# Performance work log

Hardware: AMD Instinct MI355X
Metric: run time of the kernel (lower is better)

## Reference

```python
import jax, jax.numpy as jnp
import numpy as np

N_NODES = 50000
N_EDGES = 800000
IN_DIM = 128
HID = 32
HEADS = 4
OUT_DIM = 128
NEG_SLOPE = 0.2


def setup_inputs() -> dict:
    key = jax.random.key(0)
    ks = jax.random.split(key, 10)
    s = lambda fan_in: 1.0 / np.sqrt(fan_in)
    return {
        "x": jax.random.normal(ks[0], (N_NODES, IN_DIM), dtype=jnp.float32),
        "edge_index": jax.random.randint(ks[1], (2, N_EDGES), 0, N_NODES, dtype=jnp.int64),
        # encoder GATConv: in=IN_DIM, out=HID, heads=HEADS (concat)
        "W1": jax.random.normal(ks[2], (IN_DIM, HEADS * HID), dtype=jnp.float32) * s(IN_DIM),
        "att_src1": jax.random.normal(ks[3], (HEADS, HID), dtype=jnp.float32) * s(HID),
        "att_dst1": jax.random.normal(ks[4], (HEADS, HID), dtype=jnp.float32) * s(HID),
        "b1": jnp.zeros((HEADS * HID,), dtype=jnp.float32),
        # decoder GATConv: in=HEADS*HID, out=OUT_DIM, heads=1
        "W2": jax.random.normal(ks[5], (HEADS * HID, OUT_DIM), dtype=jnp.float32) * s(HEADS * HID),
        "att_src2": jax.random.normal(ks[6], (1, OUT_DIM), dtype=jnp.float32) * s(OUT_DIM),
        "att_dst2": jax.random.normal(ks[7], (1, OUT_DIM), dtype=jnp.float32) * s(OUT_DIM),
        "b2": jnp.zeros((OUT_DIM,), dtype=jnp.float32),
    }


def _gat_conv(x, src, dst, W, att_src, att_dst, bias, heads, out_ch):
    """PyG-style GATConv (v1), eval mode (dropout off), self-loops already in src/dst."""
    n = x.shape[0]
    h = (x @ W).reshape(n, heads, out_ch)                 # [N,H,C]
    a_src = jnp.einsum("nhc,hc->nh", h, att_src)          # [N,H]
    a_dst = jnp.einsum("nhc,hc->nh", h, att_dst)          # [N,H]
    e = jax.nn.leaky_relu(a_src[src] + a_dst[dst], NEG_SLOPE)  # [E,H]
    # segment softmax over destination neighborhoods
    e_max = jax.ops.segment_max(e, dst, num_segments=n)   # [N,H]
    e_exp = jnp.exp(e - e_max[dst])
    denom = jax.ops.segment_sum(e_exp, dst, num_segments=n)
    alpha = e_exp / (denom[dst] + 1e-16)                  # [E,H]
    msg = h[src] * alpha[:, :, None]                      # [E,H,C]
    out = jax.ops.segment_sum(msg, dst, num_segments=n)   # [N,H,C]
    return out.reshape(n, heads * out_ch) + bias


def reference(x, edge_index, W1, att_src1, att_dst1, b1, W2, att_src2, att_dst2, b2):
    n = x.shape[0]
    loops = jnp.arange(n, dtype=edge_index.dtype)
    src = jnp.concatenate([edge_index[0], loops])
    dst = jnp.concatenate([edge_index[1], loops])
    z = jax.nn.relu(_gat_conv(x, src, dst, W1, att_src1, att_dst1, b1, HEADS, HID))
    x_hat = jax.nn.relu(_gat_conv(z, src, dst, W2, att_src2, att_dst2, b2, 1, OUT_DIM))
    return x_hat
```

## Files before the change

### kernel.cpp

```cpp
#include <hip/hip_runtime.h>
#include <hip/hip_bf16.h>
#include <cstddef>

#define N_NODES 50000
#define N_EDGES_RAW 800000
#define E_TOT (N_EDGES_RAW + N_NODES)
#define DIM 128
#define NEG_SLOPE 0.2f

#define NBUCK 196
#define CHUNK 4096
#define NBLK_E ((E_TOT + CHUNK - 1) / CHUNK)

typedef __attribute__((ext_vector_type(8))) short bf16x8;
typedef __attribute__((ext_vector_type(4))) float f32x4;

__device__ __forceinline__ ushort f2bf(float f) {
  unsigned u = __float_as_uint(f);
  return (ushort)((u + 0x7FFFu + ((u >> 16) & 1u)) >> 16);
}

__device__ __forceinline__ void get_edge(const int* __restrict__ ei, int is64,
                                         int e, int& s, int& d) {
  if (e >= N_EDGES_RAW) { s = e - N_EDGES_RAW; d = s; return; }
  if (is64) {
    s = ei[2 * (size_t)e];
    d = ei[2 * ((size_t)N_EDGES_RAW + (size_t)e)];
  } else {
    s = ei[e];
    d = ei[N_EDGES_RAW + e];
  }
}

__global__ void detect_i64(const int* __restrict__ ei, int* __restrict__ flag) {
  const int lane = threadIdx.x & 63;
  int hi = ei[2 * lane + 1];
  unsigned long long b = __ballot(hi != 0);
  if (lane == 0) *flag = (b == 0ULL) ? 1 : 0;
}

__global__ __launch_bounds__(256) void bucket_count(const int* __restrict__ ei,
                                                    const int* __restrict__ flag,
                                                    int* __restrict__ gbcnt) {
  __shared__ int hist[NBUCK];
  const int t = threadIdx.x;
  if (t < NBUCK) hist[t] = 0;
  __syncthreads();
  const int is64 = *flag;
  const int e0 = blockIdx.x * CHUNK;
#pragma unroll
  for (int i = 0; i < CHUNK / 256; ++i) {
    int e = e0 + i * 256 + t;
    if (e < E_TOT) {
      int s, d;
      get_edge(ei, is64, e, s, d);
      atomicAdd(&hist[d >> 8], 1);
    }
  }
  __syncthreads();
  if (t < NBUCK && hist[t] > 0) atomicAdd(&gbcnt[t], hist[t]);
}

__global__ __launch_bounds__(256) void bucket_scan(const int* __restrict__ gbcnt,
                                                   int* __restrict__ bstart,
                                                   int* __restrict__ gcur) {
  __shared__ int wtot[4];
  const int t = threadIdx.x, lane = t & 63, wid = t >> 6;
  int v = (t < NBUCK) ? gbcnt[t] : 0;
  int sc = v;
#pragma unroll
  for (int m = 1; m < 64; m <<= 1) {
    int o = __shfl_up(sc, m, 64);
    if (lane >= m) sc += o;
  }
  if (lane == 63) wtot[wid] = sc;
  __syncthreads();
  int off = 0;
  for (int w = 0; w < wid; ++w) off += wtot[w];
  int excl = off + sc - v;
  if (t < NBUCK) {
    bstart[t] = excl;
    gcur[t] = excl;
  }
  if (t == 255) bstart[NBUCK] = off + sc;
}

__global__ __launch_bounds__(256) void bucket_scatter(const int* __restrict__ ei,
                                                      const int* __restrict__ flag,
                                                      int* __restrict__ gcur,
                                                      unsigned* __restrict__ tmp) {
  __shared__ int hist[NBUCK];
  __shared__ int base[NBUCK];
  const int t = threadIdx.x;
  if (t < NBUCK) hist[t] = 0;
  __syncthreads();
  const int is64 = *flag;
  const int e0 = blockIdx.x * CHUNK;
  unsigned pair[CHUNK / 256];
  int rank[CHUNK / 256];
#pragma unroll
  for (int i = 0; i < CHUNK / 256; ++i) {
    int e = e0 + i * 256 + t;
    if (e < E_TOT) {
      int s, d;
      get_edge(ei, is64, e, s, d);
      pair[i] = (unsigned)s | ((unsigned)d << 16);
      rank[i] = atomicAdd(&hist[d >> 8], 1);
    }
  }
  __syncthreads();
  if (t < NBUCK && hist[t] > 0) base[t] = atomicAdd(&gcur[t], hist[t]);
  __syncthreads();
#pragma unroll
  for (int i = 0; i < CHUNK / 256; ++i) {
    int e = e0 + i * 256 + t;
    if (e < E_TOT) {
      int b = (int)(pair[i] >> 24);
      tmp[base[b] + rank[i]] = pair[i];
    }
  }
}

__global__ __launch_bounds__(256) void bucket_sort(const unsigned* __restrict__ tmp,
                                                   const int* __restrict__ bstart,
                                                   int* __restrict__ csr_src,
                                                   int* __restrict__ rp,
                                                   int* __restrict__ deg) {
  __shared__ int cnt[256];
  __shared__ int cur[256];
  __shared__ int wtot[4];
  const int b = blockIdx.x;
  const int t = threadIdx.x, lane = t & 63, wid = t >> 6;
  const int p0 = bstart[b], p1 = bstart[b + 1];
  cnt[t] = 0;
  __syncthreads();
  for (int j = p0 + t; j < p1; j += 256) {
    unsigned pr = tmp[j];
    atomicAdd(&cnt[(pr >> 16) & 255u], 1);
  }
  __syncthreads();
  int v = cnt[t];
  int sc = v;
#pragma unroll
  for (int m = 1; m < 64; m <<= 1) {
    int o = __shfl_up(sc, m, 64);
    if (lane >= m) sc += o;
  }
  if (lane == 63) wtot[wid] = sc;
  __syncthreads();
  int off = 0;
  for (int w = 0; w < wid; ++w) off += wtot[w];
  const int excl = off + sc - v;
  const int node = b * 256 + t;
  if (node < N_NODES) {
    deg[node] = v;
    rp[node] = p0 + excl;
  }
  cur[t] = excl;
  __syncthreads();
  for (int j = p0 + t; j < p1; j += 256) {
    unsigned pr = tmp[j];
    int ld = (int)((pr >> 16) & 255u);
    int r = atomicAdd(&cur[ld], 1);
    csr_src[p0 + r] = (int)(pr & 0xFFFFu);
  }
}

template <int H>
__global__ __launch_bounds__(256) void prep_w(const float* __restrict__ w,
                                              const float* __restrict__ atts,
                                              const float* __restrict__ attd,
                                              ushort* __restrict__ wtx) {
  const int idx = blockIdx.x * 256 + threadIdx.x;
  if (idx >= 144 * 128) return;
  const int c = idx >> 7, k = idx & 127;
  constexpr int C = 128 / H;
  float v;
  if (c < 128) {
    v = w[k * 128 + c];
  } else if (c < 128 + H) {
    const int hd = c - 128;
    float s = 0.f;
    for (int j = 0; j < C; ++j) s += w[k * 128 + hd * C + j] * atts[hd * C + j];
    v = s;
  } else if (c < 128 + 2 * H) {
    const int hd = c - 128 - H;
    float s = 0.f;
    for (int j = 0; j < C; ++j) s += w[k * 128 + hd * C + j] * attd[hd * C + j];
    v = s;
  } else {
    v = 0.f;
  }
  wtx[idx] = f2bf(v);
}

template <int H>
__global__ __launch_bounds__(256) void gemm_att(const float* __restrict__ in,
                                                const ushort* __restrict__ wtx,
                                                ushort* __restrict__ h_bf,
                                                float* __restrict__ a_src,
                                                float* __restrict__ a_dst) {
  const int wid = threadIdx.x >> 6;
  const int lane = threadIdx.x & 63;
  const int tile = blockIdx.x * 4 + wid;
  if (tile >= N_NODES / 16) return;
  const int row0 = tile * 16;
  const int rA = lane & 15;
  const int g = lane >> 4;

  f32x4 acc[9];
#pragma unroll
  for (int ct = 0; ct < 9; ++ct) acc[ct] = (f32x4){0.f, 0.f, 0.f, 0.f};

#pragma unroll
  for (int ks = 0; ks < 4; ++ks) {
    const int k0 = ks * 32 + g * 8;
    const float* ap = in + (size_t)(row0 + rA) * DIM + k0;
    float4 a0 = *(const float4*)ap;
    float4 a1 = *(const float4*)(ap + 4);
    bf16x8 af;
    af[0] = (short)f2bf(a0.x); af[1] = (short)f2bf(a0.y);
    af[2] = (short)f2bf(a0.z); af[3] = (short)f2bf(a0.w);
    af[4] = (short)f2bf(a1.x); af[5] = (short)f2bf(a1.y);
    af[6] = (short)f2bf(a1.z); af[7] = (short)f2bf(a1.w);
#pragma unroll
    for (int ct = 0; ct < 9; ++ct) {
      bf16x8 bf = *(const bf16x8*)(wtx + (size_t)(ct * 16 + rA) * 128 + k0);
      acc[ct] = __builtin_amdgcn_mfma_f32_16x16x32_bf16(af, bf, acc[ct], 0, 0, 0);
    }
  }

#pragma unroll
  for (int ct = 0; ct < 8; ++ct) {
#pragma unroll
    for (int r = 0; r < 4; ++r) {
      const int row = row0 + g * 4 + r;
      h_bf[(size_t)row * DIM + ct * 16 + rA] = f2bf(acc[ct][r]);
    }
  }
  if (rA < 2 * H) {
#pragma unroll
    for (int r = 0; r < 4; ++r) {
      const int row = row0 + g * 4 + r;
      if (rA < H)
        a_src[(size_t)row * H + rA] = acc[8][r];
      else
        a_dst[(size_t)row * H + (rA - H)] = acc[8][r];
    }
  }
}

template <int H>
__global__ __launch_bounds__(256) void node_agg(const int* __restrict__ rp,
                                                const int* __restrict__ deg,
                                                const int* __restrict__ csr_src,
                                                const ushort* __restrict__ h_bf,
                                                const float* __restrict__ a_src,
                                                const float* __restrict__ a_dst,
                                                const float* __restrict__ bias,
                                                float* __restrict__ outp) {
  const int wid = threadIdx.x >> 6;
  const int lane = threadIdx.x & 63;
  const int node = blockIdx.x * 4 + wid;
  if (node >= N_NODES) return;
  constexpr int LPH = (DIM / H) / 2;
  const int head = lane / LPH;
  const float ad = a_dst[(size_t)node * H + head];
  const int beg = rp[node];
  const int dg = deg[node];
  const int* __restrict__ srcs = csr_src + beg;

  float sden = 0.f, ax = 0.f, ay = 0.f;
#pragma unroll 4
  for (int j = 0; j < dg; ++j) {
    int s = srcs[j];
    float v = a_src[(size_t)s * H + head] + ad;
    v = v > 0.f ? v : NEG_SLOPE * v;
    v = fminf(fmaxf(v, -60.f), 80.f);
    float p = __expf(v);
    uint hv = ((const uint*)(h_bf + (size_t)s * DIM))[lane];
    float hx = __uint_as_float((hv & 0xFFFFu) << 16);
    float hy = __uint_as_float(hv & 0xFFFF0000u);
    sden += p;
    ax += p * hx;
    ay += p * hy;
  }
  const float inv = 1.f / sden;
  float2 bv = ((const float2*)bias)[lane];
  float ox = fmaxf(ax * inv + bv.x, 0.f);
  float oy = fmaxf(ay * inv + bv.y, 0.f);
  ((float2*)(outp + (size_t)node * DIM))[lane] = make_float2(ox, oy);
}

extern "C" void kernel_launch(void* const* d_in, const int* in_sizes, int n_in,
                              void* d_out, int out_size, void* d_ws, size_t ws_size,
                              hipStream_t stream) {
  const float* x   = (const float*)d_in[0];
  const int*   ei  = (const int*)d_in[1];
  const float* W1  = (const float*)d_in[2];
  const float* as1 = (const float*)d_in[3];
  const float* ad1 = (const float*)d_in[4];
  const float* b1  = (const float*)d_in[5];
  const float* W2  = (const float*)d_in[6];
  const float* as2 = (const float*)d_in[7];
  const float* ad2 = (const float*)d_in[8];
  const float* b2  = (const float*)d_in[9];
  float* out = (float*)d_out;

  float* ws = (float*)d_ws;
  const size_t F_H = (size_t)N_NODES * DIM;
  float*    z      = ws;
  ushort*   h_bf   = (ushort*)(z + F_H);
  float*    a_src  = z + F_H + F_H / 2;
  float*    a_dst  = a_src + 200000;
  int*      deg    = (int*)(a_dst + 200000);
  int*      rp     = deg + N_NODES;
  int*      csr_src= rp + N_NODES;
  unsigned* tmp    = (unsigned*)(csr_src + E_TOT);
  int*      gbcnt  = (int*)(tmp + E_TOT);
  int*      bstart = gbcnt + 256;
  int*      gcur   = bstart + 256;
  int*      flag   = gcur + 256;
  ushort*   wtx1   = (ushort*)(flag + 4);
  ushort*   wtx2   = wtx1 + 144 * 128;

  const int GB = (N_NODES / 16 + 3) / 4;

  hipLaunchKernelGGL(detect_i64, dim3(1), dim3(64), 0, stream, ei, flag);
  hipMemsetAsync(gbcnt, 0, NBUCK * sizeof(int), stream);
  hipLaunchKernelGGL((prep_w<4>), dim3(72), dim3(256), 0, stream, W1, as1, ad1, wtx1);
  hipLaunchKernelGGL((prep_w<1>), dim3(72), dim3(256), 0, stream, W2, as2, ad2, wtx2);
  hipLaunchKernelGGL(bucket_count, dim3(NBLK_E), dim3(256), 0, stream, ei, flag, gbcnt);
  hipLaunchKernelGGL(bucket_scan, dim3(1), dim3(256), 0, stream, gbcnt, bstart, gcur);
  hipLaunchKernelGGL(bucket_scatter, dim3(NBLK_E), dim3(256), 0, stream, ei, flag, gcur, tmp);
  hipLaunchKernelGGL(bucket_sort, dim3(NBUCK), dim3(256), 0, stream,
                     tmp, bstart, csr_src, rp, deg);

  hipLaunchKernelGGL((gemm_att<4>), dim3(GB), dim3(256), 0, stream,
                     x, wtx1, h_bf, a_src, a_dst);
  hipLaunchKernelGGL((node_agg<4>), dim3((N_NODES + 3) / 4), dim3(256), 0, stream,
                     rp, deg, csr_src, h_bf, a_src, a_dst, b1, z);

  hipLaunchKernelGGL((gemm_att<1>), dim3(GB), dim3(256), 0, stream,
                     z, wtx2, h_bf, a_src, a_dst);
  hipLaunchKernelGGL((node_agg<1>), dim3((N_NODES + 3) / 4), dim3(256), 0, stream,
                     rp, deg, csr_src, h_bf, a_src, a_dst, b2, out);
}
```

Baseline: 195.8 us.

## Process two edges per wavefront in aggregation and merge setup launches

The node aggregation kernel now splits each wavefront into two 32-lane halves that handle alternate neighbors. Each lane loads four bf16 features (uint2) instead of two, and the halves are combined with a cross-half shuffle at the end. This doubles the number of independent gathers in flight per node and halves the loop trip count. Separately, the int64 detection, weight preparation and counter memset are folded into a single setup kernel plus inline detection, which removes several small launches at the cost of every bucket block re-reading the detection words.

```diff
diff --git a/kernel.cpp b/kernel.cpp
--- a/kernel.cpp
+++ b/kernel.cpp
@@ -32,149 +32,25 @@
   }
 }
 
-__global__ void detect_i64(const int* __restrict__ ei, int* __restrict__ flag) {
-  const int lane = threadIdx.x & 63;
-  int hi = ei[2 * lane + 1];
-  unsigned long long b = __ballot(hi != 0);
-  if (lane == 0) *flag = (b == 0ULL) ? 1 : 0;
-}
-
-__global__ __launch_bounds__(256) void bucket_count(const int* __restrict__ ei,
-                                                    const int* __restrict__ flag,
-                                                    int* __restrict__ gbcnt) {
-  __shared__ int hist[NBUCK];
+__device__ __forceinline__ int detect_inline(const int* __restrict__ ei,
+                                             int* sflag) {
   const int t = threadIdx.x;
-  if (t < NBUCK) hist[t] = 0;
-  __syncthreads();
-  const int is64 = *flag;
-  const int e0 = blockIdx.x * CHUNK;
-#pragma unroll
-  for (int i = 0; i < CHUNK / 256; ++i) {
-    int e = e0 + i * 256 + t;
-    if (e < E_TOT) {
-      int s, d;
-      get_edge(ei, is64, e, s, d);
-      atomicAdd(&hist[d >> 8], 1);
-    }
-  }
-  __syncthreads();
-  if (t < NBUCK && hist[t] > 0) atomicAdd(&gbcnt[t], hist[t]);
-}
-
-__global__ __launch_bounds__(256) void bucket_scan(const int* __restrict__ gbcnt,
-                                                   int* __restrict__ bstart,
-                                                   int* __restrict__ gcur) {
-  __shared__ int wtot[4];
-  const int t = threadIdx.x, lane = t & 63, wid = t >> 6;
-  int v = (t < NBUCK) ? gbcnt[t] : 0;
-  int sc = v;
-#pragma unroll
-  for (int m = 1; m < 64; m <<= 1) {
-    int o = __shfl_up(sc, m, 64);
-    if (lane >= m) sc += o;
-  }
-  if (lane == 63) wtot[wid] = sc;
-  __syncthreads();
-  int off = 0;
-  for (int w = 0; w < wid; ++w) off += wtot[w];
-  int excl = off + sc - v;
-  if (t < NBUCK) {
-    bstart[t] = excl;
-    gcur[t] = excl;
-  }
-  if (t == 255) bstart[NBUCK] = off + sc;
-}
-
-__global__ __launch_bounds__(256) void bucket_scatter(const int* __restrict__ ei,
-                                                      const int* __restrict__ flag,
-                                                      int* __restrict__ gcur,
-                                                      unsigned* __restrict__ tmp) {
-  __shared__ int hist[NBUCK];
-  __shared__ int base[NBUCK];
-  const int t = threadIdx.x;
-  if (t < NBUCK) hist[t] = 0;
-  __syncthreads();
-  const int is64 = *flag;
-  const int e0 = blockIdx.x * CHUNK;
-  unsigned pair[CHUNK / 256];
-  int rank[CHUNK / 256];
-#pragma unroll
-  for (int i = 0; i < CHUNK / 256; ++i) {
-    int e = e0 + i * 256 + t;
-    if (e < E_TOT) {
-      int s, d;
-      get_edge(ei, is64, e, s, d);
-      pair[i] = (unsigned)s | ((unsigned)d << 16);
-      rank[i] = atomicAdd(&hist[d >> 8], 1);
-    }
-  }
-  __syncthreads();
-  if (t < NBUCK && hist[t] > 0) base[t] = atomicAdd(&gcur[t], hist[t]);
-  __syncthreads();
-#pragma unroll
-  for (int i = 0; i < CHUNK / 256; ++i) {
-    int e = e0 + i * 256 + t;
-    if (e < E_TOT) {
-      int b = (int)(pair[i] >> 24);
-      tmp[base[b] + rank[i]] = pair[i];
-    }
-  }
-}
-
-__global__ __launch_bounds__(256) void bucket_sort(const unsigned* __restrict__ tmp,
-                                                   const int* __restrict__ bstart,
-                                                   int* __restrict__ csr_src,
-                                                   int* __restrict__ rp,
-                                                   int* __restrict__ deg) {
-  __shared__ int cnt[256];
-  __shared__ int cur[256];
-  __shared__ int wtot[4];
-  const int b = blockIdx.x;
-  const int t = threadIdx.x, lane = t & 63, wid = t >> 6;
-  const int p0 = bstart[b], p1 = bstart[b + 1];
-  cnt[t] = 0;
-  __syncthreads();
-  for (int j = p0 + t; j < p1; j += 256) {
-    unsigned pr = tmp[j];
-    atomicAdd(&cnt[(pr >> 16) & 255u], 1);
-  }
-  __syncthreads();
-  int v = cnt[t];
-  int sc = v;
-#pragma unroll
-  for (int m = 1; m < 64; m <<= 1) {
-    int o = __shfl_up(sc, m, 64);
-    if (lane >= m) sc += o;
-  }
-  if (lane == 63) wtot[wid] = sc;
-  __syncthreads();
-  int off = 0;
-  for (int w = 0; w < wid; ++w) off += wtot[w];
-  const int excl = off + sc - v;
-  const int node = b * 256 + t;
-  if (node < N_NODES) {
-    deg[node] = v;
-    rp[node] = p0 + excl;
-  }
-  cur[t] = excl;
-  __syncthreads();
-  for (int j = p0 + t; j < p1; j += 256) {
-    unsigned pr = tmp[j];
-    int ld = (int)((pr >> 16) & 255u);
-    int r = atomicAdd(&cur[ld], 1);
-    csr_src[p0 + r] = (int)(pr & 0xFFFFu);
-  }
-}
-
-template <int H>
-__global__ __launch_bounds__(256) void prep_w(const float* __restrict__ w,
-                                              const float* __restrict__ atts,
-                                              const float* __restrict__ attd,
-                                              ushort* __restrict__ wtx) {
-  const int idx = blockIdx.x * 256 + threadIdx.x;
-  if (idx >= 144 * 128) return;
+  if (t < 64) {
+    int hi = ei[2 * t + 1];
+    unsigned long long b = __ballot(hi != 0);
+    if (t == 0) *sflag = (b == 0ULL) ? 1 : 0;
+  }
+  __syncthreads();
+  return *sflag;
+}
+
+__device__ __forceinline__ void prep_one(const float* __restrict__ w,
+                                         const float* __restrict__ atts,
+                                         const float* __restrict__ attd,
+                                         ushort* __restrict__ wtx,
+                                         int H, int idx) {
   const int c = idx >> 7, k = idx & 127;
-  constexpr int C = 128 / H;
+  const int C = 128 / H;
   float v;
   if (c < 128) {
     v = w[k * 128 + c];
@@ -194,6 +70,152 @@
   wtx[idx] = f2bf(v);
 }
 
+__global__ __launch_bounds__(256) void setup(const float* __restrict__ W1,
+                                             const float* __restrict__ as1,
+                                             const float* __restrict__ ad1,
+                                             ushort* __restrict__ wtx1,
+                                             const float* __restrict__ W2,
+                                             const float* __restrict__ as2,
+                                             const float* __restrict__ ad2,
+                                             ushort* __restrict__ wtx2,
+                                             int* __restrict__ gbcnt) {
+  const int b = blockIdx.x, t = threadIdx.x;
+  if (b < 72) {
+    prep_one(W1, as1, ad1, wtx1, 4, b * 256 + t);
+  } else if (b < 144) {
+    prep_one(W2, as2, ad2, wtx2, 1, (b - 72) * 256 + t);
+  } else {
+    if (t < NBUCK) gbcnt[t] = 0;
+  }
+}
+
+__global__ __launch_bounds__(256) void bucket_count(const int* __restrict__ ei,
+                                                    int* __restrict__ gbcnt) {
+  __shared__ int hist[NBUCK];
+  __shared__ int sflag;
+  const int t = threadIdx.x;
+  if (t < NBUCK) hist[t] = 0;
+  const int is64 = detect_inline(ei, &sflag);
+  __syncthreads();
+  const int e0 = blockIdx.x * CHUNK;
+#pragma unroll
+  for (int i = 0; i < CHUNK / 256; ++i) {
+    int e = e0 + i * 256 + t;
+    if (e < E_TOT) {
+      int s, d;
+      get_edge(ei, is64, e, s, d);
+      atomicAdd(&hist[d >> 8], 1);
+    }
+  }
+  __syncthreads();
+  if (t < NBUCK && hist[t] > 0) atomicAdd(&gbcnt[t], hist[t]);
+}
+
+__global__ __launch_bounds__(256) void bucket_scan(const int* __restrict__ gbcnt,
+                                                   int* __restrict__ bstart,
+                                                   int* __restrict__ gcur) {
+  __shared__ int wtot[4];
+  const int t = threadIdx.x, lane = t & 63, wid = t >> 6;
+  int v = (t < NBUCK) ? gbcnt[t] : 0;
+  int sc = v;
+#pragma unroll
+  for (int m = 1; m < 64; m <<= 1) {
+    int o = __shfl_up(sc, m, 64);
+    if (lane >= m) sc += o;
+  }
+  if (lane == 63) wtot[wid] = sc;
+  __syncthreads();
+  int off = 0;
+  for (int w = 0; w < wid; ++w) off += wtot[w];
+  int excl = off + sc - v;
+  if (t < NBUCK) {
+    bstart[t] = excl;
+    gcur[t] = excl;
+  }
+  if (t == 255) bstart[NBUCK] = off + sc;
+}
+
+__global__ __launch_bounds__(256) void bucket_scatter(const int* __restrict__ ei,
+                                                      int* __restrict__ gcur,
+                                                      unsigned* __restrict__ tmp) {
+  __shared__ int hist[NBUCK];
+  __shared__ int base[NBUCK];
+  __shared__ int sflag;
+  const int t = threadIdx.x;
+  if (t < NBUCK) hist[t] = 0;
+  const int is64 = detect_inline(ei, &sflag);
+  __syncthreads();
+  const int e0 = blockIdx.x * CHUNK;
+  unsigned pair[CHUNK / 256];
+  int rank[CHUNK / 256];
+#pragma unroll
+  for (int i = 0; i < CHUNK / 256; ++i) {
+    int e = e0 + i * 256 + t;
+    if (e < E_TOT) {
+      int s, d;
+      get_edge(ei, is64, e, s, d);
+      pair[i] = (unsigned)s | ((unsigned)d << 16);
+      rank[i] = atomicAdd(&hist[d >> 8], 1);
+    }
+  }
+  __syncthreads();
+  if (t < NBUCK && hist[t] > 0) base[t] = atomicAdd(&gcur[t], hist[t]);
+  __syncthreads();
+#pragma unroll
+  for (int i = 0; i < CHUNK / 256; ++i) {
+    int e = e0 + i * 256 + t;
+    if (e < E_TOT) {
+      int b = (int)(pair[i] >> 24);
+      tmp[base[b] + rank[i]] = pair[i];
+    }
+  }
+}
+
+__global__ __launch_bounds__(256) void bucket_sort(const unsigned* __restrict__ tmp,
+                                                   const int* __restrict__ bstart,
+                                                   int* __restrict__ csr_src,
+                                                   int* __restrict__ rp,
+                                                   int* __restrict__ deg) {
+  __shared__ int cnt[256];
+  __shared__ int cur[256];
+  __shared__ int wtot[4];
+  const int b = blockIdx.x;
+  const int t = threadIdx.x, lane = t & 63, wid = t >> 6;
+  const int p0 = bstart[b], p1 = bstart[b + 1];
+  cnt[t] = 0;
+  __syncthreads();
+  for (int j = p0 + t; j < p1; j += 256) {
+    unsigned pr = tmp[j];
+    atomicAdd(&cnt[(pr >> 16) & 255u], 1);
+  }
+  __syncthreads();
+  int v = cnt[t];
+  int sc = v;
+#pragma unroll
+  for (int m = 1; m < 64; m <<= 1) {
+    int o = __shfl_up(sc, m, 64);
+    if (lane >= m) sc += o;
+  }
+  if (lane == 63) wtot[wid] = sc;
+  __syncthreads();
+  int off = 0;
+  for (int w = 0; w < wid; ++w) off += wtot[w];
+  const int excl = off + sc - v;
+  const int node = b * 256 + t;
+  if (node < N_NODES) {
+    deg[node] = v;
+    rp[node] = p0 + excl;
+  }
+  cur[t] = excl;
+  __syncthreads();
+  for (int j = p0 + t; j < p1; j += 256) {
+    unsigned pr = tmp[j];
+    int ld = (int)((pr >> 16) & 255u);
+    int r = atomicAdd(&cur[ld], 1);
+    csr_src[p0 + r] = (int)(pr & 0xFFFFu);
+  }
+}
+
 template <int H>
 __global__ __launch_bounds__(256) void gemm_att(const float* __restrict__ in,
                                                 const ushort* __restrict__ wtx,
@@ -263,33 +285,64 @@
   const int lane = threadIdx.x & 63;
   const int node = blockIdx.x * 4 + wid;
   if (node >= N_NODES) return;
-  constexpr int LPH = (DIM / H) / 2;
-  const int head = lane / LPH;
+  const int hl = lane & 31;
+  const int head = (H == 4) ? (hl >> 3) : 0;
   const float ad = a_dst[(size_t)node * H + head];
   const int beg = rp[node];
   const int dg = deg[node];
   const int* __restrict__ srcs = csr_src + beg;
 
-  float sden = 0.f, ax = 0.f, ay = 0.f;
-#pragma unroll 4
-  for (int j = 0; j < dg; ++j) {
-    int s = srcs[j];
+  float sden = 0.f;
+  float a0 = 0.f, a1 = 0.f, a2 = 0.f, a3 = 0.f;
+
+  const int dg2 = dg & ~1;
+#pragma unroll 2
+  for (int j = 0; j < dg2; j += 2) {
+    int s = srcs[j + (lane >> 5)];
     float v = a_src[(size_t)s * H + head] + ad;
     v = v > 0.f ? v : NEG_SLOPE * v;
     v = fminf(fmaxf(v, -60.f), 80.f);
     float p = __expf(v);
-    uint hv = ((const uint*)(h_bf + (size_t)s * DIM))[lane];
-    float hx = __uint_as_float((hv & 0xFFFFu) << 16);
-    float hy = __uint_as_float(hv & 0xFFFF0000u);
+    uint2 hv = ((const uint2*)(h_bf + (size_t)s * DIM))[hl];
+    float h0 = __uint_as_float((hv.x & 0xFFFFu) << 16);
+    float h1 = __uint_as_float(hv.x & 0xFFFF0000u);
+    float h2 = __uint_as_float((hv.y & 0xFFFFu) << 16);
+    float h3 = __uint_as_float(hv.y & 0xFFFF0000u);
     sden += p;
-    ax += p * hx;
-    ay += p * hy;
-  }
-  const float inv = 1.f / sden;
-  float2 bv = ((const float2*)bias)[lane];
-  float ox = fmaxf(ax * inv + bv.x, 0.f);
-  float oy = fmaxf(ay * inv + bv.y, 0.f);
-  ((float2*)(outp + (size_t)node * DIM))[lane] = make_float2(ox, oy);
+    a0 += p * h0; a1 += p * h1; a2 += p * h2; a3 += p * h3;
+  }
+  if (dg & 1) {
+    int s = srcs[dg - 1];
+    float v = a_src[(size_t)s * H + head] + ad;
+    v = v > 0.f ? v : NEG_SLOPE * v;
+    v = fminf(fmaxf(v, -60.f), 80.f);
+    float p = __expf(v);
+    if (lane >= 32) p = 0.f;
+    uint2 hv = ((const uint2*)(h_bf + (size_t)s * DIM))[hl];
+    float h0 = __uint_as_float((hv.x & 0xFFFFu) << 16);
+    float h1 = __uint_as_float(hv.x & 0xFFFF0000u);
+    float h2 = __uint_as_float((hv.y & 0xFFFFu) << 16);
+    float h3 = __uint_as_float(hv.y & 0xFFFF0000u);
+    sden += p;
+    a0 += p * h0; a1 += p * h1; a2 += p * h2; a3 += p * h3;
+  }
+
+  sden += __shfl_xor(sden, 32);
+  a0 += __shfl_xor(a0, 32);
+  a1 += __shfl_xor(a1, 32);
+  a2 += __shfl_xor(a2, 32);
+  a3 += __shfl_xor(a3, 32);
+
+  if (lane < 32) {
+    const float inv = 1.f / sden;
+    float4 bv = ((const float4*)bias)[hl];
+    float4 o;
+    o.x = fmaxf(a0 * inv + bv.x, 0.f);
+    o.y = fmaxf(a1 * inv + bv.y, 0.f);
+    o.z = fmaxf(a2 * inv + bv.z, 0.f);
+    o.w = fmaxf(a3 * inv + bv.w, 0.f);
+    ((float4*)(outp + (size_t)node * DIM))[hl] = o;
+  }
 }
 
 extern "C" void kernel_launch(void* const* d_in, const int* in_sizes, int n_in,
@@ -320,19 +373,16 @@
   int*      gbcnt  = (int*)(tmp + E_TOT);
   int*      bstart = gbcnt + 256;
   int*      gcur   = bstart + 256;
-  int*      flag   = gcur + 256;
-  ushort*   wtx1   = (ushort*)(flag + 4);
+  ushort*   wtx1   = (ushort*)(gcur + 256);
   ushort*   wtx2   = wtx1 + 144 * 128;
 
   const int GB = (N_NODES / 16 + 3) / 4;
 
-  hipLaunchKernelGGL(detect_i64, dim3(1), dim3(64), 0, stream, ei, flag);
-  hipMemsetAsync(gbcnt, 0, NBUCK * sizeof(int), stream);
-  hipLaunchKernelGGL((prep_w<4>), dim3(72), dim3(256), 0, stream, W1, as1, ad1, wtx1);
-  hipLaunchKernelGGL((prep_w<1>), dim3(72), dim3(256), 0, stream, W2, as2, ad2, wtx2);
-  hipLaunchKernelGGL(bucket_count, dim3(NBLK_E), dim3(256), 0, stream, ei, flag, gbcnt);
+  hipLaunchKernelGGL(setup, dim3(145), dim3(256), 0, stream,
+                     W1, as1, ad1, wtx1, W2, as2, ad2, wtx2, gbcnt);
+  hipLaunchKernelGGL(bucket_count, dim3(NBLK_E), dim3(256), 0, stream, ei, gbcnt);
   hipLaunchKernelGGL(bucket_scan, dim3(1), dim3(256), 0, stream, gbcnt, bstart, gcur);
-  hipLaunchKernelGGL(bucket_scatter, dim3(NBLK_E), dim3(256), 0, stream, ei, flag, gcur, tmp);
+  hipLaunchKernelGGL(bucket_scatter, dim3(NBLK_E), dim3(256), 0, stream, ei, gcur, tmp);
   hipLaunchKernelGGL(bucket_sort, dim3(NBUCK), dim3(256), 0, stream,
                      tmp, bstart, csr_src, rp, deg);
 
```

New measurement: 178.3 us. 1.1x faster.
